# Performance work log

Hardware: AMD Instinct MI355X
Metric: run time of the kernel (lower is better)

Reference implementation:

```python
import jax, jax.numpy as jnp
import numpy as np


def setup_inputs() -> dict:
    key = jax.random.key(0)
    k1, k2, k3, k4, k5 = jax.random.split(key, 5)
    b, c, k, h, w = 8, 512, 19, 128, 128
    x = jax.random.normal(k1, (b, c, h, w), dtype=jnp.float32)
    # mask_conv: 1x1 conv ichn->ochn (weight [k, c], bias [k])
    Wm = jax.random.normal(k2, (k, c), dtype=jnp.float32) * (1.0 / np.sqrt(c))
    bm = jax.random.normal(k3, (k,), dtype=jnp.float32) * 0.02
    # filter_conv: grouped 1x1 conv, groups=k -> per-class [c_out, c_in] matmul
    Wf = jax.random.normal(k4, (k, c, c), dtype=jnp.float32) * (1.0 / np.sqrt(c))
    bf = jax.random.normal(k5, (k, c), dtype=jnp.float32) * 0.02
    return {"x": x, "Wm": Wm, "bm": bm, "Wf": Wf, "bf": bf}


def reference(x, Wm, bm, Wf, bf):
    b, c, h, w = x.shape
    k = Wm.shape[0]
    # mask_conv (1x1) + sigmoid -> [b, k, h, w]
    pre_mask = jnp.einsum('bchw,kc->bkhw', x, Wm) + bm[None, :, None, None]
    mask = jax.nn.sigmoid(pre_mask)
    # masked pooling: bmm(mask [b,k,hw], feat [b,hw,c]) / (h*w) -> [b, k, c]
    class_feat = jnp.einsum('bkhw,bchw->bkc', mask, x) / (h * w)
    # grouped 1x1 filter_conv: per class k, [c_out, c_in] GEMM on class_feat
    filters = jnp.einsum('koc,bkc->bko', Wf, class_feat) + bf[None, :, :]  # [b, k, c]
    # per-sample dynamic 1x1 conv (groups=b) == batched GEMM over channels
    pred = jnp.einsum('bkc,bchw->bkhw', filters, x)
    return pred
```

## Files before the change

kernel.cpp:

```cpp
#include <hip/hip_runtime.h>
#include <math.h>

#define BB 8
#define CC 512
#define KK 19
#define HWHW 16384
#define INV_HW (1.0f/16384.0f)

typedef __attribute__((ext_vector_type(8))) short bf16x8;
typedef __attribute__((ext_vector_type(4))) short s16x4;
typedef __attribute__((ext_vector_type(4))) float f32x4;

__device__ __forceinline__ unsigned short f2bf(float f) {
    unsigned int u = __float_as_uint(f);
    u = (u + 0x7fffu + ((u >> 16) & 1u)) >> 16;
    return (unsigned short)u;
}

__global__ __launch_bounds__(256) void k_s1(const float* __restrict__ x,
                                            const float* __restrict__ Wm,
                                            const float* __restrict__ bm,
                                            unsigned short* __restrict__ mask) {
    __shared__ short wm[20 * CC];
    __shared__ short xt[128 * 64];
    const int tid = threadIdx.x;
    const int b = blockIdx.x >> 7;
    const int p0 = (blockIdx.x & 127) << 7;
    const float* xb = x + ((size_t)b * CC) * HWHW + p0;

    for (int u = tid; u < 20 * 128; u += 256) {
        const int k = u >> 7;
        const int c4 = (u & 127) << 2;
        float4 w = {0.f, 0.f, 0.f, 0.f};
        if (k < KK) w = *(const float4*)(Wm + k * CC + c4);
        s16x4 v = { (short)f2bf(w.x), (short)f2bf(w.y), (short)f2bf(w.z), (short)f2bf(w.w) };
        *(s16x4*)&wm[(k << 9) + (((c4 >> 3) ^ (k & 7)) << 3) + (c4 & 7)] = v;
    }

    const int wv = tid >> 6, ln = tid & 63;
    const int lm = ln & 15, q = ln >> 4;
    const f32x4 zz = {0.f, 0.f, 0.f, 0.f};
    f32x4 acc[2][2];
    acc[0][0] = zz; acc[0][1] = zz; acc[1][0] = zz; acc[1][1] = zz;

    for (int cs = 0; cs < 8; ++cs) {
        __syncthreads();
#pragma unroll
        for (int r = 0; r < 2; ++r) {
            const int u = tid + (r << 8);
            const int cg = u >> 5;
            const int p = (u & 31) << 2;
            const float* src = xb + (size_t)((cs << 6) + (cg << 2)) * HWHW + p;
            float4 F0 = *(const float4*)(src);
            float4 F1 = *(const float4*)(src + HWHW);
            float4 F2 = *(const float4*)(src + 2 * HWHW);
            float4 F3 = *(const float4*)(src + 3 * HWHW);
            const float* G0 = (const float*)&F0;
            const float* G1 = (const float*)&F1;
            const float* G2 = (const float*)&F2;
            const float* G3 = (const float*)&F3;
#pragma unroll
            for (int j = 0; j < 4; ++j) {
                const int pr = p + j;
                s16x4 v = { (short)f2bf(G0[j]), (short)f2bf(G1[j]),
                            (short)f2bf(G2[j]), (short)f2bf(G3[j]) };
                *(s16x4*)&xt[(pr << 6) + (((cg >> 1) ^ (pr & 7)) << 3) + ((cg & 1) << 2)] = v;
            }
        }
        __syncthreads();
#pragma unroll
        for (int ks = 0; ks < 2; ++ks) {
            const int gch = (cs << 3) + (ks << 2) + q;
            const int m1 = (lm < 3) ? (16 + lm) : 19;
            bf16x8 a0 = *(const bf16x8*)&wm[(lm << 9) + ((gch ^ (lm & 7)) << 3)];
            bf16x8 a1 = *(const bf16x8*)&wm[(m1 << 9) + ((gch ^ (m1 & 7)) << 3)];
            const int lch = (ks << 2) + q;
#pragma unroll
            for (int nt = 0; nt < 2; ++nt) {
                const int pr = (((wv << 1) + nt) << 4) + lm;
                bf16x8 bf_ = *(const bf16x8*)&xt[(pr << 6) + ((lch ^ (pr & 7)) << 3)];
                acc[0][nt] = __builtin_amdgcn_mfma_f32_16x16x32_bf16(a0, bf_, acc[0][nt], 0, 0, 0);
                acc[1][nt] = __builtin_amdgcn_mfma_f32_16x16x32_bf16(a1, bf_, acc[1][nt], 0, 0, 0);
            }
        }
    }

    unsigned short* mb = mask + ((size_t)b * KK) * HWHW + p0;
#pragma unroll
    for (int mt = 0; mt < 2; ++mt)
#pragma unroll
        for (int r = 0; r < 4; ++r) {
            const int k = (mt << 4) + (q << 2) + r;
            if (k < KK) {
                const float bias = bm[k];
#pragma unroll
                for (int nt = 0; nt < 2; ++nt) {
                    const int p = (((wv << 1) + nt) << 4) + lm;
                    const float t = acc[mt][nt][r] + bias;
                    mb[(size_t)k * HWHW + p] = f2bf(1.0f / (1.0f + __expf(-t)));
                }
            }
        }
}

__global__ __launch_bounds__(256) void k_s2(const float* __restrict__ x,
                                            const unsigned short* __restrict__ mask,
                                            float* __restrict__ cf_part) {
    __shared__ short mt_[20 * 64];
    __shared__ short xtl[64 * 64];
    const int tid = threadIdx.x;
    const int s = blockIdx.x & 15;
    const int ct = (blockIdx.x >> 4) & 7;
    const int b = blockIdx.x >> 7;
    const int wv = tid >> 6, ln = tid & 63;
    const int lm = ln & 15, q = ln >> 4;
    const float* xb = x + ((size_t)b * CC + (ct << 6)) * HWHW + (s << 10);
    const unsigned short* mbs = mask + ((size_t)b * KK) * HWHW + (s << 10);

    const f32x4 zz = {0.f, 0.f, 0.f, 0.f};
    f32x4 acc[2];
    acc[0] = zz; acc[1] = zz;

    for (int kp = 0; kp < 16; ++kp) {
        __syncthreads();
        if (tid < 160) {
            const int k = tid >> 3, ch = tid & 7;
            uint4 v = {0u, 0u, 0u, 0u};
            if (k < KK) v = *(const uint4*)(mbs + (size_t)k * HWHW + (kp << 6) + (ch << 3));
            *(uint4*)&mt_[(k << 6) + ((ch ^ (k & 7)) << 3)] = v;
        }
#pragma unroll
        for (int r = 0; r < 4; ++r) {
            const int u = tid + (r << 8);
            const int c = u >> 4;
            const int pq = u & 15;
            float4 f = *(const float4*)(xb + (size_t)c * HWHW + (kp << 6) + (pq << 2));
            s16x4 v = { (short)f2bf(f.x), (short)f2bf(f.y), (short)f2bf(f.z), (short)f2bf(f.w) };
            *(s16x4*)&xtl[(c << 6) + (((pq >> 1) ^ (c & 7)) << 3) + ((pq & 1) << 2)] = v;
        }
        __syncthreads();
#pragma unroll
        for (int ks = 0; ks < 2; ++ks) {
            const int pch = (ks << 2) + q;
            const int cr = (wv << 4) + lm;
            bf16x8 bf_ = *(const bf16x8*)&xtl[(cr << 6) + ((pch ^ (cr & 7)) << 3)];
            const int m1 = (lm < 3) ? (16 + lm) : 19;
            bf16x8 a0 = *(const bf16x8*)&mt_[(lm << 6) + ((pch ^ (lm & 7)) << 3)];
            bf16x8 a1 = *(const bf16x8*)&mt_[(m1 << 6) + ((pch ^ (m1 & 7)) << 3)];
            acc[0] = __builtin_amdgcn_mfma_f32_16x16x32_bf16(a0, bf_, acc[0], 0, 0, 0);
            acc[1] = __builtin_amdgcn_mfma_f32_16x16x32_bf16(a1, bf_, acc[1], 0, 0, 0);
        }
    }

    float* dst = cf_part + ((size_t)(s * BB + b) * KK) * CC + (ct << 6) + (wv << 4) + lm;
#pragma unroll
    for (int mt = 0; mt < 2; ++mt)
#pragma unroll
        for (int r = 0; r < 4; ++r) {
            const int k = (mt << 4) + (q << 2) + r;
            if (k < KK) dst[(size_t)k * CC] = acc[mt][r];
        }
}

__global__ __launch_bounds__(256) void k_s2r(const float* __restrict__ part,
                                             float* __restrict__ cf) {
    const int i = blockIdx.x * 256 + threadIdx.x;
    if (i >= BB * KK * CC) return;
    const int b = i / (KK * CC);
    const int rem = i - b * (KK * CC);
    float sum = 0.0f;
#pragma unroll
    for (int s = 0; s < 16; ++s)
        sum += part[((size_t)(s * BB + b) * KK) * CC + rem];
    cf[i] = sum * INV_HW;
}

__global__ __launch_bounds__(256) void k_filters(const float* __restrict__ Wf,
                                                 const float* __restrict__ bf,
                                                 const float* __restrict__ cf,
                                                 float* __restrict__ fil) {
    const int blk = blockIdx.x;
    const int k = blk >> 7;
    const int o = ((blk & 127) << 2) + (threadIdx.x >> 6);
    const int lane = threadIdx.x & 63;
    const float* wrow = Wf + ((size_t)k * CC + o) * CC;

    float acc[BB];
#pragma unroll
    for (int b = 0; b < BB; ++b) acc[b] = 0.0f;
#pragma unroll
    for (int j = 0; j < CC / 64; ++j) {
        const int c = lane + (j << 6);
        const float wv = wrow[c];
#pragma unroll
        for (int b = 0; b < BB; ++b)
            acc[b] += wv * cf[((size_t)b * KK + k) * CC + c];
    }
#pragma unroll
    for (int b = 0; b < BB; ++b) {
#pragma unroll
        for (int off = 32; off > 0; off >>= 1)
            acc[b] += __shfl_down(acc[b], off, 64);
    }
    if (lane == 0) {
        const float bias = bf[k * CC + o];
#pragma unroll
        for (int b = 0; b < BB; ++b)
            fil[((size_t)b * KK + k) * CC + o] = acc[b] + bias;
    }
}

__global__ __launch_bounds__(256) void k_s4(const float* __restrict__ x,
                                            const float* __restrict__ fil,
                                            float* __restrict__ out) {
    __shared__ short wm[20 * CC];
    __shared__ short xt[128 * 64];
    const int tid = threadIdx.x;
    const int b = blockIdx.x >> 7;
    const int p0 = (blockIdx.x & 127) << 7;
    const float* xb = x + ((size_t)b * CC) * HWHW + p0;
    const float* fb = fil + ((size_t)b * KK) * CC;

    for (int u = tid; u < 20 * 128; u += 256) {
        const int k = u >> 7;
        const int c4 = (u & 127) << 2;
        float4 w = {0.f, 0.f, 0.f, 0.f};
        if (k < KK) w = *(const float4*)(fb + k * CC + c4);
        s16x4 v = { (short)f2bf(w.x), (short)f2bf(w.y), (short)f2bf(w.z), (short)f2bf(w.w) };
        *(s16x4*)&wm[(k << 9) + (((c4 >> 3) ^ (k & 7)) << 3) + (c4 & 7)] = v;
    }

    const int wv = tid >> 6, ln = tid & 63;
    const int lm = ln & 15, q = ln >> 4;
    const f32x4 zz = {0.f, 0.f, 0.f, 0.f};
    f32x4 acc[2][2];
    acc[0][0] = zz; acc[0][1] = zz; acc[1][0] = zz; acc[1][1] = zz;

    for (int cs = 0; cs < 8; ++cs) {
        __syncthreads();
#pragma unroll
        for (int r = 0; r < 2; ++r) {
            const int u = tid + (r << 8);
            const int cg = u >> 5;
            const int p = (u & 31) << 2;
            const float* src = xb + (size_t)((cs << 6) + (cg << 2)) * HWHW + p;
            float4 F0 = *(const float4*)(src);
            float4 F1 = *(const float4*)(src + HWHW);
            float4 F2 = *(const float4*)(src + 2 * HWHW);
            float4 F3 = *(const float4*)(src + 3 * HWHW);
            const float* G0 = (const float*)&F0;
            const float* G1 = (const float*)&F1;
            const float* G2 = (const float*)&F2;
            const float* G3 = (const float*)&F3;
#pragma unroll
            for (int j = 0; j < 4; ++j) {
                const int pr = p + j;
                s16x4 v = { (short)f2bf(G0[j]), (short)f2bf(G1[j]),
                            (short)f2bf(G2[j]), (short)f2bf(G3[j]) };
                *(s16x4*)&xt[(pr << 6) + (((cg >> 1) ^ (pr & 7)) << 3) + ((cg & 1) << 2)] = v;
            }
        }
        __syncthreads();
#pragma unroll
        for (int ks = 0; ks < 2; ++ks) {
            const int gch = (cs << 3) + (ks << 2) + q;
            const int m1 = (lm < 3) ? (16 + lm) : 19;
            bf16x8 a0 = *(const bf16x8*)&wm[(lm << 9) + ((gch ^ (lm & 7)) << 3)];
            bf16x8 a1 = *(const bf16x8*)&wm[(m1 << 9) + ((gch ^ (m1 & 7)) << 3)];
            const int lch = (ks << 2) + q;
#pragma unroll
            for (int nt = 0; nt < 2; ++nt) {
                const int pr = (((wv << 1) + nt) << 4) + lm;
                bf16x8 bf_ = *(const bf16x8*)&xt[(pr << 6) + ((lch ^ (pr & 7)) << 3)];
                acc[0][nt] = __builtin_amdgcn_mfma_f32_16x16x32_bf16(a0, bf_, acc[0][nt], 0, 0, 0);
                acc[1][nt] = __builtin_amdgcn_mfma_f32_16x16x32_bf16(a1, bf_, acc[1][nt], 0, 0, 0);
            }
        }
    }

    float* ob = out + ((size_t)b * KK) * HWHW + p0;
#pragma unroll
    for (int mt = 0; mt < 2; ++mt)
#pragma unroll
        for (int r = 0; r < 4; ++r) {
            const int k = (mt << 4) + (q << 2) + r;
            if (k < KK) {
#pragma unroll
                for (int nt = 0; nt < 2; ++nt) {
                    const int p = (((wv << 1) + nt) << 4) + lm;
                    ob[(size_t)k * HWHW + p] = acc[mt][nt][r];
                }
            }
        }
}

extern "C" void kernel_launch(void* const* d_in, const int* in_sizes, int n_in,
                              void* d_out, int out_size, void* d_ws, size_t ws_size,
                              hipStream_t stream) {
    const float* x  = (const float*)d_in[0];
    const float* Wm = (const float*)d_in[1];
    const float* bm = (const float*)d_in[2];
    const float* Wf = (const float*)d_in[3];
    const float* bf = (const float*)d_in[4];
    float* out = (float*)d_out;

    unsigned short* mask = (unsigned short*)d_ws;
    float* cf_part = (float*)((char*)d_ws + (size_t)BB * KK * HWHW * 2);
    float* cf  = cf_part + (size_t)16 * BB * KK * CC;
    float* fil = cf + (size_t)BB * KK * CC;

    k_s1<<<1024, 256, 0, stream>>>(x, Wm, bm, mask);
    k_s2<<<1024, 256, 0, stream>>>(x, mask, cf_part);
    k_s2r<<<(BB * KK * CC + 255) / 256, 256, 0, stream>>>(cf_part, cf);
    k_filters<<<KK * 128, 256, 0, stream>>>(Wf, bf, cf, fil);
    k_s4<<<1024, 256, 0, stream>>>(x, fil, out);
}
```

Baseline: 476.2 us.

## Enlarge pixel tiles and let pooling blocks cover all channels

The mask and output GEMM kernels now give each block 256 pixels instead of 128, loading 8 channels per thread and writing 16-byte LDS stores with a new XOR swizzle. The pooling kernel is restructured so each block handles all 512 channels over a 256-pixel slice, loading the mask tile once per block instead of once per channel tile. The per-slice partials grow from 16 to 64, so the reduction kernel reads more data. The grids halve to 512 blocks and the larger LDS tiles and accumulator arrays (64 KB in pooling) lower occupancy.

```diff
diff --git a/kernel.cpp b/kernel.cpp
--- a/kernel.cpp
+++ b/kernel.cpp
@@ -7,14 +7,16 @@
 #define HWHW 16384
 #define INV_HW (1.0f/16384.0f)
 
+#define SWZ(r) ((((r) ^ ((r) >> 2))) & 7)
+
 typedef __attribute__((ext_vector_type(8))) short bf16x8;
 typedef __attribute__((ext_vector_type(4))) short s16x4;
 typedef __attribute__((ext_vector_type(4))) float f32x4;
 
-__device__ __forceinline__ unsigned short f2bf(float f) {
+__device__ __forceinline__ short f2bf(float f) {
     unsigned int u = __float_as_uint(f);
     u = (u + 0x7fffu + ((u >> 16) & 1u)) >> 16;
-    return (unsigned short)u;
+    return (short)u;
 }
 
 __global__ __launch_bounds__(256) void k_s1(const float* __restrict__ x,
@@ -22,10 +24,10 @@
                                             const float* __restrict__ bm,
                                             unsigned short* __restrict__ mask) {
     __shared__ short wm[20 * CC];
-    __shared__ short xt[128 * 64];
+    __shared__ short xt[256 * 64];
     const int tid = threadIdx.x;
-    const int b = blockIdx.x >> 7;
-    const int p0 = (blockIdx.x & 127) << 7;
+    const int b = blockIdx.x >> 6;
+    const int p0 = (blockIdx.x & 63) << 8;
     const float* xb = x + ((size_t)b * CC) * HWHW + p0;
 
     for (int u = tid; u < 20 * 128; u += 256) {
@@ -33,54 +35,52 @@
         const int c4 = (u & 127) << 2;
         float4 w = {0.f, 0.f, 0.f, 0.f};
         if (k < KK) w = *(const float4*)(Wm + k * CC + c4);
-        s16x4 v = { (short)f2bf(w.x), (short)f2bf(w.y), (short)f2bf(w.z), (short)f2bf(w.w) };
-        *(s16x4*)&wm[(k << 9) + (((c4 >> 3) ^ (k & 7)) << 3) + (c4 & 7)] = v;
+        s16x4 v = { f2bf(w.x), f2bf(w.y), f2bf(w.z), f2bf(w.w) };
+        const int chunk = c4 >> 3, half = (c4 >> 2) & 1;
+        *(s16x4*)&wm[(k << 9) + ((chunk ^ SWZ(k)) << 3) + (half << 2)] = v;
     }
 
     const int wv = tid >> 6, ln = tid & 63;
     const int lm = ln & 15, q = ln >> 4;
+    const int m1 = (lm < 3) ? (16 + lm) : 19;
     const f32x4 zz = {0.f, 0.f, 0.f, 0.f};
-    f32x4 acc[2][2];
-    acc[0][0] = zz; acc[0][1] = zz; acc[1][0] = zz; acc[1][1] = zz;
+    f32x4 acc[2][4];
+#pragma unroll
+    for (int i = 0; i < 4; ++i) { acc[0][i] = zz; acc[1][i] = zz; }
 
     for (int cs = 0; cs < 8; ++cs) {
         __syncthreads();
 #pragma unroll
         for (int r = 0; r < 2; ++r) {
             const int u = tid + (r << 8);
-            const int cg = u >> 5;
-            const int p = (u & 31) << 2;
-            const float* src = xb + (size_t)((cs << 6) + (cg << 2)) * HWHW + p;
-            float4 F0 = *(const float4*)(src);
-            float4 F1 = *(const float4*)(src + HWHW);
-            float4 F2 = *(const float4*)(src + 2 * HWHW);
-            float4 F3 = *(const float4*)(src + 3 * HWHW);
-            const float* G0 = (const float*)&F0;
-            const float* G1 = (const float*)&F1;
-            const float* G2 = (const float*)&F2;
-            const float* G3 = (const float*)&F3;
+            const int cg8 = u >> 6;
+            const int p = (u & 63) << 2;
+            const float* src = xb + (size_t)((cs << 6) + (cg8 << 3)) * HWHW + p;
+            float4 F[8];
+#pragma unroll
+            for (int i = 0; i < 8; ++i) F[i] = *(const float4*)(src + (size_t)i * HWHW);
+            const float* G = (const float*)F;
 #pragma unroll
             for (int j = 0; j < 4; ++j) {
                 const int pr = p + j;
-                s16x4 v = { (short)f2bf(G0[j]), (short)f2bf(G1[j]),
-                            (short)f2bf(G2[j]), (short)f2bf(G3[j]) };
-                *(s16x4*)&xt[(pr << 6) + (((cg >> 1) ^ (pr & 7)) << 3) + ((cg & 1) << 2)] = v;
+                bf16x8 v = { f2bf(G[0*4+j]), f2bf(G[1*4+j]), f2bf(G[2*4+j]), f2bf(G[3*4+j]),
+                             f2bf(G[4*4+j]), f2bf(G[5*4+j]), f2bf(G[6*4+j]), f2bf(G[7*4+j]) };
+                *(bf16x8*)&xt[(pr << 6) + ((cg8 ^ SWZ(pr)) << 3)] = v;
             }
         }
         __syncthreads();
 #pragma unroll
         for (int ks = 0; ks < 2; ++ks) {
             const int gch = (cs << 3) + (ks << 2) + q;
-            const int m1 = (lm < 3) ? (16 + lm) : 19;
-            bf16x8 a0 = *(const bf16x8*)&wm[(lm << 9) + ((gch ^ (lm & 7)) << 3)];
-            bf16x8 a1 = *(const bf16x8*)&wm[(m1 << 9) + ((gch ^ (m1 & 7)) << 3)];
+            bf16x8 a0 = *(const bf16x8*)&wm[(lm << 9) + ((gch ^ SWZ(lm)) << 3)];
+            bf16x8 a1 = *(const bf16x8*)&wm[(m1 << 9) + ((gch ^ SWZ(m1)) << 3)];
             const int lch = (ks << 2) + q;
 #pragma unroll
-            for (int nt = 0; nt < 2; ++nt) {
-                const int pr = (((wv << 1) + nt) << 4) + lm;
-                bf16x8 bf_ = *(const bf16x8*)&xt[(pr << 6) + ((lch ^ (pr & 7)) << 3)];
-                acc[0][nt] = __builtin_amdgcn_mfma_f32_16x16x32_bf16(a0, bf_, acc[0][nt], 0, 0, 0);
-                acc[1][nt] = __builtin_amdgcn_mfma_f32_16x16x32_bf16(a1, bf_, acc[1][nt], 0, 0, 0);
+            for (int nt = 0; nt < 4; ++nt) {
+                const int pr = (((wv << 2) + nt) << 4) + lm;
+                bf16x8 bfr = *(const bf16x8*)&xt[(pr << 6) + ((lch ^ SWZ(pr)) << 3)];
+                acc[0][nt] = __builtin_amdgcn_mfma_f32_16x16x32_bf16(a0, bfr, acc[0][nt], 0, 0, 0);
+                acc[1][nt] = __builtin_amdgcn_mfma_f32_16x16x32_bf16(a1, bfr, acc[1][nt], 0, 0, 0);
             }
         }
     }
@@ -94,10 +94,10 @@
             if (k < KK) {
                 const float bias = bm[k];
 #pragma unroll
-                for (int nt = 0; nt < 2; ++nt) {
-                    const int p = (((wv << 1) + nt) << 4) + lm;
+                for (int nt = 0; nt < 4; ++nt) {
+                    const int p = (((wv << 2) + nt) << 4) + lm;
                     const float t = acc[mt][nt][r] + bias;
-                    mb[(size_t)k * HWHW + p] = f2bf(1.0f / (1.0f + __expf(-t)));
+                    mb[(size_t)k * HWHW + p] = (unsigned short)f2bf(1.0f / (1.0f + __expf(-t)));
                 }
             }
         }
@@ -107,58 +107,73 @@
                                             const unsigned short* __restrict__ mask,
                                             float* __restrict__ cf_part) {
     __shared__ short mt_[20 * 64];
-    __shared__ short xtl[64 * 64];
+    __shared__ short xtl[512 * 64];
     const int tid = threadIdx.x;
-    const int s = blockIdx.x & 15;
-    const int ct = (blockIdx.x >> 4) & 7;
-    const int b = blockIdx.x >> 7;
+    const int b = blockIdx.x >> 6;
+    const int s = blockIdx.x & 63;
     const int wv = tid >> 6, ln = tid & 63;
     const int lm = ln & 15, q = ln >> 4;
-    const float* xb = x + ((size_t)b * CC + (ct << 6)) * HWHW + (s << 10);
-    const unsigned short* mbs = mask + ((size_t)b * KK) * HWHW + (s << 10);
+    const int m1 = (lm < 3) ? (16 + lm) : 19;
+    const float* xb = x + ((size_t)b * CC) * HWHW + (s << 8);
+    const unsigned short* mbs = mask + ((size_t)b * KK) * HWHW + (s << 8);
 
     const f32x4 zz = {0.f, 0.f, 0.f, 0.f};
-    f32x4 acc[2];
-    acc[0] = zz; acc[1] = zz;
-
-    for (int kp = 0; kp < 16; ++kp) {
+    f32x4 acc[2][8];
+#pragma unroll
+    for (int i = 0; i < 8; ++i) { acc[0][i] = zz; acc[1][i] = zz; }
+
+    for (int kp = 0; kp < 4; ++kp) {
         __syncthreads();
         if (tid < 160) {
             const int k = tid >> 3, ch = tid & 7;
             uint4 v = {0u, 0u, 0u, 0u};
             if (k < KK) v = *(const uint4*)(mbs + (size_t)k * HWHW + (kp << 6) + (ch << 3));
-            *(uint4*)&mt_[(k << 6) + ((ch ^ (k & 7)) << 3)] = v;
+            *(uint4*)&mt_[(k << 6) + ((ch ^ SWZ(k)) << 3)] = v;
         }
 #pragma unroll
         for (int r = 0; r < 4; ++r) {
             const int u = tid + (r << 8);
-            const int c = u >> 4;
+            const int cg8 = u >> 4;
             const int pq = u & 15;
-            float4 f = *(const float4*)(xb + (size_t)c * HWHW + (kp << 6) + (pq << 2));
-            s16x4 v = { (short)f2bf(f.x), (short)f2bf(f.y), (short)f2bf(f.z), (short)f2bf(f.w) };
-            *(s16x4*)&xtl[(c << 6) + (((pq >> 1) ^ (c & 7)) << 3) + ((pq & 1) << 2)] = v;
+            const int p = pq << 2;
+            const float* src = xb + (size_t)(cg8 << 3) * HWHW + (kp << 6) + p;
+#pragma unroll
+            for (int i = 0; i < 8; ++i) {
+                float4 f = *(const float4*)(src + (size_t)i * HWHW);
+                const int c = (cg8 << 3) + i;
+                s16x4 v = { f2bf(f.x), f2bf(f.y), f2bf(f.z), f2bf(f.w) };
+                *(s16x4*)&xtl[(c << 6) + (((pq >> 1) ^ SWZ(c)) << 3) + ((pq & 1) << 2)] = v;
+            }
         }
         __syncthreads();
 #pragma unroll
         for (int ks = 0; ks < 2; ++ks) {
             const int pch = (ks << 2) + q;
-            const int cr = (wv << 4) + lm;
-            bf16x8 bf_ = *(const bf16x8*)&xtl[(cr << 6) + ((pch ^ (cr & 7)) << 3)];
-            const int m1 = (lm < 3) ? (16 + lm) : 19;
-            bf16x8 a0 = *(const bf16x8*)&mt_[(lm << 6) + ((pch ^ (lm & 7)) << 3)];
-            bf16x8 a1 = *(const bf16x8*)&mt_[(m1 << 6) + ((pch ^ (m1 & 7)) << 3)];
-            acc[0] = __builtin_amdgcn_mfma_f32_16x16x32_bf16(a0, bf_, acc[0], 0, 0, 0);
-            acc[1] = __builtin_amdgcn_mfma_f32_16x16x32_bf16(a1, bf_, acc[1], 0, 0, 0);
-        }
-    }
-
-    float* dst = cf_part + ((size_t)(s * BB + b) * KK) * CC + (ct << 6) + (wv << 4) + lm;
+            bf16x8 a0 = *(const bf16x8*)&mt_[(lm << 6) + ((pch ^ SWZ(lm)) << 3)];
+            bf16x8 a1 = *(const bf16x8*)&mt_[(m1 << 6) + ((pch ^ SWZ(m1)) << 3)];
+#pragma unroll
+            for (int nt = 0; nt < 8; ++nt) {
+                const int c = (((wv << 3) + nt) << 4) + lm;
+                bf16x8 bfr = *(const bf16x8*)&xtl[(c << 6) + ((pch ^ SWZ(c)) << 3)];
+                acc[0][nt] = __builtin_amdgcn_mfma_f32_16x16x32_bf16(a0, bfr, acc[0][nt], 0, 0, 0);
+                acc[1][nt] = __builtin_amdgcn_mfma_f32_16x16x32_bf16(a1, bfr, acc[1][nt], 0, 0, 0);
+            }
+        }
+    }
+
+    float* dst = cf_part + ((size_t)((s << 3) + b) * KK) * CC;
 #pragma unroll
     for (int mt = 0; mt < 2; ++mt)
 #pragma unroll
         for (int r = 0; r < 4; ++r) {
             const int k = (mt << 4) + (q << 2) + r;
-            if (k < KK) dst[(size_t)k * CC] = acc[mt][r];
+            if (k < KK) {
+#pragma unroll
+                for (int nt = 0; nt < 8; ++nt) {
+                    const int c = (((wv << 3) + nt) << 4) + lm;
+                    dst[(size_t)k * CC + c] = acc[mt][nt][r];
+                }
+            }
         }
 }
 
@@ -170,8 +185,8 @@
     const int rem = i - b * (KK * CC);
     float sum = 0.0f;
 #pragma unroll
-    for (int s = 0; s < 16; ++s)
-        sum += part[((size_t)(s * BB + b) * KK) * CC + rem];
+    for (int s = 0; s < 64; ++s)
+        sum += part[((size_t)((s << 3) + b) * KK) * CC + rem];
     cf[i] = sum * INV_HW;
 }
 
@@ -214,10 +229,10 @@
                                             const float* __restrict__ fil,
                                             float* __restrict__ out) {
     __shared__ short wm[20 * CC];
-    __shared__ short xt[128 * 64];
+    __shared__ short xt[256 * 64];
     const int tid = threadIdx.x;
-    const int b = blockIdx.x >> 7;
-    const int p0 = (blockIdx.x & 127) << 7;
+    const int b = blockIdx.x >> 6;
+    const int p0 = (blockIdx.x & 63) << 8;
     const float* xb = x + ((size_t)b * CC) * HWHW + p0;
     const float* fb = fil + ((size_t)b * KK) * CC;
 
@@ -226,54 +241,52 @@
         const int c4 = (u & 127) << 2;
         float4 w = {0.f, 0.f, 0.f, 0.f};
         if (k < KK) w = *(const float4*)(fb + k * CC + c4);
-        s16x4 v = { (short)f2bf(w.x), (short)f2bf(w.y), (short)f2bf(w.z), (short)f2bf(w.w) };
-        *(s16x4*)&wm[(k << 9) + (((c4 >> 3) ^ (k & 7)) << 3) + (c4 & 7)] = v;
+        s16x4 v = { f2bf(w.x), f2bf(w.y), f2bf(w.z), f2bf(w.w) };
+        const int chunk = c4 >> 3, half = (c4 >> 2) & 1;
+        *(s16x4*)&wm[(k << 9) + ((chunk ^ SWZ(k)) << 3) + (half << 2)] = v;
     }
 
     const int wv = tid >> 6, ln = tid & 63;
     const int lm = ln & 15, q = ln >> 4;
+    const int m1 = (lm < 3) ? (16 + lm) : 19;
     const f32x4 zz = {0.f, 0.f, 0.f, 0.f};
-    f32x4 acc[2][2];
-    acc[0][0] = zz; acc[0][1] = zz; acc[1][0] = zz; acc[1][1] = zz;
+    f32x4 acc[2][4];
+#pragma unroll
+    for (int i = 0; i < 4; ++i) { acc[0][i] = zz; acc[1][i] = zz; }
 
     for (int cs = 0; cs < 8; ++cs) {
         __syncthreads();
 #pragma unroll
         for (int r = 0; r < 2; ++r) {
             const int u = tid + (r << 8);
-            const int cg = u >> 5;
-            const int p = (u & 31) << 2;
-            const float* src = xb + (size_t)((cs << 6) + (cg << 2)) * HWHW + p;
-            float4 F0 = *(const float4*)(src);
-            float4 F1 = *(const float4*)(src + HWHW);
-            float4 F2 = *(const float4*)(src + 2 * HWHW);
-            float4 F3 = *(const float4*)(src + 3 * HWHW);
-            const float* G0 = (const float*)&F0;
-            const float* G1 = (const float*)&F1;
-            const float* G2 = (const float*)&F2;
-            const float* G3 = (const float*)&F3;
+            const int cg8 = u >> 6;
+            const int p = (u & 63) << 2;
+            const float* src = xb + (size_t)((cs << 6) + (cg8 << 3)) * HWHW + p;
+            float4 F[8];
+#pragma unroll
+            for (int i = 0; i < 8; ++i) F[i] = *(const float4*)(src + (size_t)i * HWHW);
+            const float* G = (const float*)F;
 #pragma unroll
             for (int j = 0; j < 4; ++j) {
                 const int pr = p + j;
-                s16x4 v = { (short)f2bf(G0[j]), (short)f2bf(G1[j]),
-                            (short)f2bf(G2[j]), (short)f2bf(G3[j]) };
-                *(s16x4*)&xt[(pr << 6) + (((cg >> 1) ^ (pr & 7)) << 3) + ((cg & 1) << 2)] = v;
+                bf16x8 v = { f2bf(G[0*4+j]), f2bf(G[1*4+j]), f2bf(G[2*4+j]), f2bf(G[3*4+j]),
+                             f2bf(G[4*4+j]), f2bf(G[5*4+j]), f2bf(G[6*4+j]), f2bf(G[7*4+j]) };
+                *(bf16x8*)&xt[(pr << 6) + ((cg8 ^ SWZ(pr)) << 3)] = v;
             }
         }
         __syncthreads();
 #pragma unroll
         for (int ks = 0; ks < 2; ++ks) {
             const int gch = (cs << 3) + (ks << 2) + q;
-            const int m1 = (lm < 3) ? (16 + lm) : 19;
-            bf16x8 a0 = *(const bf16x8*)&wm[(lm << 9) + ((gch ^ (lm & 7)) << 3)];
-            bf16x8 a1 = *(const bf16x8*)&wm[(m1 << 9) + ((gch ^ (m1 & 7)) << 3)];
+            bf16x8 a0 = *(const bf16x8*)&wm[(lm << 9) + ((gch ^ SWZ(lm)) << 3)];
+            bf16x8 a1 = *(const bf16x8*)&wm[(m1 << 9) + ((gch ^ SWZ(m1)) << 3)];
             const int lch = (ks << 2) + q;
 #pragma unroll
-            for (int nt = 0; nt < 2; ++nt) {
-                const int pr = (((wv << 1) + nt) << 4) + lm;
-                bf16x8 bf_ = *(const bf16x8*)&xt[(pr << 6) + ((lch ^ (pr & 7)) << 3)];
-                acc[0][nt] = __builtin_amdgcn_mfma_f32_16x16x32_bf16(a0, bf_, acc[0][nt], 0, 0, 0);
-                acc[1][nt] = __builtin_amdgcn_mfma_f32_16x16x32_bf16(a1, bf_, acc[1][nt], 0, 0, 0);
+            for (int nt = 0; nt < 4; ++nt) {
+                const int pr = (((wv << 2) + nt) << 4) + lm;
+                bf16x8 bfr = *(const bf16x8*)&xt[(pr << 6) + ((lch ^ SWZ(pr)) << 3)];
+                acc[0][nt] = __builtin_amdgcn_mfma_f32_16x16x32_bf16(a0, bfr, acc[0][nt], 0, 0, 0);
+                acc[1][nt] = __builtin_amdgcn_mfma_f32_16x16x32_bf16(a1, bfr, acc[1][nt], 0, 0, 0);
             }
         }
     }
@@ -286,8 +299,8 @@
             const int k = (mt << 4) + (q << 2) + r;
             if (k < KK) {
 #pragma unroll
-                for (int nt = 0; nt < 2; ++nt) {
-                    const int p = (((wv << 1) + nt) << 4) + lm;
+                for (int nt = 0; nt < 4; ++nt) {
+                    const int p = (((wv << 2) + nt) << 4) + lm;
                     ob[(size_t)k * HWHW + p] = acc[mt][nt][r];
                 }
             }
@@ -306,12 +319,12 @@
 
     unsigned short* mask = (unsigned short*)d_ws;
     float* cf_part = (float*)((char*)d_ws + (size_t)BB * KK * HWHW * 2);
-    float* cf  = cf_part + (size_t)16 * BB * KK * CC;
+    float* cf  = cf_part + (size_t)64 * BB * KK * CC;
     float* fil = cf + (size_t)BB * KK * CC;
 
-    k_s1<<<1024, 256, 0, stream>>>(x, Wm, bm, mask);
-    k_s2<<<1024, 256, 0, stream>>>(x, mask, cf_part);
+    k_s1<<<512, 256, 0, stream>>>(x, Wm, bm, mask);
+    k_s2<<<512, 256, 0, stream>>>(x, mask, cf_part);
     k_s2r<<<(BB * KK * CC + 255) / 256, 256, 0, stream>>>(cf_part, cf);
     k_filters<<<KK * 128, 256, 0, stream>>>(Wf, bf, cf, fil);
-    k_s4<<<1024, 256, 0, stream>>>(x, fil, out);
-}
+    k_s4<<<512, 256, 0, stream>>>(x, fil, out);
+}
```

New measurement: 499.8 us. +5.0%, slower.
